# Kernel tuning notes

Measured on AMD Instinct MI355X. Metric: run time of the kernel, lower is better.

Reference implementation:

```python
import jax, jax.numpy as jnp
import numpy as np

RADIUS = 1.0
N_NORM = 1  # default n_norm in the torch module


def setup_inputs() -> dict:
    key = jax.random.key(0)
    k1, k2, k3 = jax.random.split(key, 3)
    batch, n, c_in, c_out = 8, 2048, 64, 64
    features = jax.random.normal(k1, (batch, n, c_in), dtype=jnp.float32)
    geometry = jax.random.normal(k2, (batch, n, 3), dtype=jnp.float32)
    # learned per-edge kernel weight: K(diff)[o,i] = sum_x diff[x] * Wk[x,o,i]
    Wk = jax.random.normal(k3, (3, c_out, c_in), dtype=jnp.float32) * 0.1
    return {"features": features, "geometry": geometry, "Wk": Wk}


def reference(features, geometry, Wk):
    # diff[z,a,b,:] = geometry[z,b] - geometry[z,a]   (rb - ra in the torch code)
    diff = geometry[:, None, :, :] - geometry[:, :, None, :]  # [z, a, b, 3]
    norm = jnp.sqrt(jnp.sum(diff * diff, axis=-1))            # [z, a, b]
    # Dense masked formulation: padding every point's neighbor list to k = n
    # with rel_mask zeros is mathematically identical to the torch variable-k
    # padding (masked entries contribute nothing to the einsum reduce).
    rel_mask = (norm < RADIUS).astype(features.dtype)         # [z, a, b]
    # Fused reduce. Original: einsum('zab,zabij,zabj->zai', mask, K(diff), feat[nei])
    # with K(diff)[z,a,b,i,j] = einsum('zabx,xij->zabij', diff, Wk). We contract
    # over b first to avoid materializing the [z,a,b,i,j] kernel tensor.
    s = jnp.einsum('zab,zabx,zbj->zaxj', rel_mask, diff, features)  # [z, a, 3, c_in]
    out = jnp.einsum('zaxj,xij->zai', s, Wk) / jnp.sqrt(jnp.asarray(N_NORM, features.dtype))
    return out
```

## Files before the change

kernel.cpp:

```cpp
#include <hip/hip_runtime.h>
#include <stdint.h>

#define NPTS 2048

#define BP_OFF    0ULL
#define BP_BYTES  (8ULL * 8 * 64 * 2 * 1024)
#define W2F_OFF   (BP_OFF + BP_BYTES)
#define W2F_BYTES (24ULL * 1024)
#define WXF_OFF   (W2F_OFF + W2F_BYTES)
#define WXF_BYTES (24ULL * 1024)
#define MW_OFF    (WXF_OFF + WXF_BYTES)
#define MW_BYTES  (8ULL * 32 * 64 * 256)

typedef __attribute__((ext_vector_type(8))) short bf16x8;
typedef __attribute__((ext_vector_type(4))) float f32x4;
typedef __attribute__((ext_vector_type(16))) float f32x16;
typedef __attribute__((ext_vector_type(4))) unsigned int u32x4;

__device__ __forceinline__ unsigned f2bf(float f) {
  union { float f; unsigned u; } v; v.f = f;
  return (v.u + 0x7FFFu + ((v.u >> 16) & 1u)) >> 16;
}

__device__ __forceinline__ bf16x8 pack8(const float4 a, const float4 b) {
  u32x4 r;
  r[0] = f2bf(a.x) | (f2bf(a.y) << 16);
  r[1] = f2bf(a.z) | (f2bf(a.w) << 16);
  r[2] = f2bf(b.x) | (f2bf(b.y) << 16);
  r[3] = f2bf(b.z) | (f2bf(b.w) << 16);
  union { u32x4 u; bf16x8 h; } c; c.u = r; return c.h;
}

__device__ __forceinline__ bf16x8 unpack_mask(unsigned mq) {
  const unsigned dep0 = ((mq & 15u) * 0x204081u) & 0x01010101u;
  const unsigned dep1 = (((mq >> 4) & 15u) * 0x204081u) & 0x01010101u;
  u32x4 aw;
  aw[0] = __builtin_amdgcn_perm(dep0, 0u, 0x0C050C04u) * 0x3F80u;
  aw[1] = __builtin_amdgcn_perm(dep0, 0u, 0x0C070C06u) * 0x3F80u;
  aw[2] = __builtin_amdgcn_perm(dep1, 0u, 0x0C050C04u) * 0x3F80u;
  aw[3] = __builtin_amdgcn_perm(dep1, 0u, 0x0C070C06u) * 0x3F80u;
  union { u32x4 u; bf16x8 h; } cv; cv.u = aw;
  return cv.h;
}

__global__ __launch_bounds__(256, 2) void k1_prep(const float* __restrict__ feat,
                                                  const float* __restrict__ geom,
                                                  const float* __restrict__ Wk,
                                                  unsigned char* __restrict__ ws) {
  const int blk = blockIdx.x, t = threadIdx.x;
  if (blk < 512) {
    const int z = blk >> 6, s = blk & 63;
    __shared__ float FT[64][37];
    __shared__ float g[96];
    __shared__ float gxp[2048], gyp[2048], gzp[2048];
    const float* fz = feat + ((size_t)z * NPTS + s * 32) * 64;
    const float* gz = geom + (size_t)z * NPTS * 3;
    {
      const int row = t >> 3, j0 = (t & 7) << 3;
      const float4 v0 = *(const float4*)&fz[row * 64 + j0];
      const float4 v1 = *(const float4*)&fz[row * 64 + j0 + 4];
      FT[j0 + 0][row] = v0.x; FT[j0 + 1][row] = v0.y;
      FT[j0 + 2][row] = v0.z; FT[j0 + 3][row] = v0.w;
      FT[j0 + 4][row] = v1.x; FT[j0 + 5][row] = v1.y;
      FT[j0 + 6][row] = v1.z; FT[j0 + 7][row] = v1.w;
    }
    if (t < 96) g[t] = gz[s * 96 + t];
    {
      float v[24];
#pragma unroll
      for (int i = 0; i < 6; ++i) *(float4*)&v[i * 4] = *(const float4*)&gz[t * 24 + i * 4];
#pragma unroll
      for (int i = 0; i < 8; ++i) {
        const int pp = i * 256 + t;
        gxp[pp] = v[i * 3 + 0]; gyp[pp] = v[i * 3 + 1]; gzp[pp] = v[i * 3 + 2];
      }
    }
    __syncthreads();

    {
      const int w = t >> 6, L = t & 63;
      const int nn = L >> 2, k0 = (L & 3) * 8;
      const int j = w * 16 + nn;
      float f[8];
#pragma unroll
      for (int i = 0; i < 8; ++i) f[i] = FT[j][k0 + i];
      float gx[3][8];
#pragma unroll
      for (int x = 0; x < 3; ++x)
#pragma unroll
        for (int i = 0; i < 8; ++i) gx[x][i] = g[(k0 + i) * 3 + x];
      const int kc = (L & 3) >> 1, h = (L & 3) & 1;
      const int lane16 = h * 32 + (w & 1) * 16 + nn;
      unsigned char* base = ws + BP_OFF + (size_t)z * 1048576 + (size_t)(w >> 1) * 131072 +
                            (size_t)s * 2048 + (size_t)kc * 1024 + (size_t)lane16 * 16;
#pragma unroll
      for (int it = 0; it < 4; ++it) {
        u32x4 pv;
#pragma unroll
        for (int p = 0; p < 4; ++p) {
          float f0 = f[2 * p], f1 = f[2 * p + 1];
          if (it < 3) { f0 *= gx[it][2 * p]; f1 *= gx[it][2 * p + 1]; }
          pv[p] = f2bf(f0) | (f2bf(f1) << 16);
        }
        *(u32x4*)(base + (size_t)it * 262144) = pv;
      }
    }

    {
      float ax[8], ay[8], az[8];
#pragma unroll
      for (int i = 0; i < 8; ++i) {
        const int pp = i * 256 + t;
        ax[i] = gxp[pp]; ay[i] = gyp[pp]; az[i] = gzp[pp];
      }
      unsigned bits[8] = {0, 0, 0, 0, 0, 0, 0, 0};
      for (int j = 0; j < 32; ++j) {
        const float bx = g[j * 3 + 0], by = g[j * 3 + 1], bz = g[j * 3 + 2];
#pragma unroll
        for (int i = 0; i < 8; ++i) {
          const float d0 = bx - ax[i], d1 = by - ay[i], d2 = bz - az[i];
          const float n2 = fmaf(d2, d2, fmaf(d1, d1, d0 * d0));
          bits[i] |= (n2 < 1.0f ? 1u : 0u) << j;
        }
      }
      unsigned int* mw = (unsigned int*)(ws + MW_OFF);
#pragma unroll
      for (int i = 0; i < 8; ++i) {
        const int r = t * 8 + i;
        mw[(((size_t)z * 32 + (r >> 6)) * 64 + s) * 64 + (r & 15) * 4 + ((r >> 4) & 3)] = bits[i];
      }
    }
  } else if (blk == 512) {
    for (int e = t; e < 1536; e += 256) {
      const int frag = e >> 6, lp = e & 63, nn = lp >> 2, qd = lp & 3;
      const int kb = frag >> 2, cb = frag & 3;
      u32x4 pv;
#pragma unroll
      for (int p = 0; p < 4; ++p) {
        const int k0 = kb * 32 + qd * 8 + 2 * p;
        const float v0 = Wk[(k0 >> 6) * 4096 + (cb * 16 + nn) * 64 + (k0 & 63)];
        const float v1 = Wk[((k0 + 1) >> 6) * 4096 + (cb * 16 + nn) * 64 + ((k0 + 1) & 63)];
        pv[p] = f2bf(v0) | (f2bf(v1) << 16);
      }
      *(u32x4*)(ws + W2F_OFF + (size_t)frag * 1024 + lp * 16) = pv;
    }
  } else {
    for (int e = t; e < 1536; e += 256) {
      const int frag = e >> 6, lp = e & 63, nn = lp >> 2, qd = lp & 3;
      const int kb = frag / 12, cb = frag % 12, xi = cb * 16 + nn;
      u32x4 pv;
#pragma unroll
      for (int p = 0; p < 4; ++p) {
        const int k0 = kb * 32 + qd * 8 + 2 * p;
        const float v0 = Wk[(xi >> 6) * 4096 + (xi & 63) * 64 + k0];
        const float v1 = Wk[(xi >> 6) * 4096 + (xi & 63) * 64 + k0 + 1];
        pv[p] = f2bf(v0) | (f2bf(v1) << 16);
      }
      *(u32x4*)(ws + WXF_OFF + (size_t)frag * 1024 + lp * 16) = pv;
    }
  }
}

__global__ __launch_bounds__(512, 2) void k2_gemm(const float* __restrict__ geom,
                                                  const unsigned char* __restrict__ ws,
                                                  float* __restrict__ out) {
  __shared__ __align__(16) float Ct[64 * 256];

  const int t = threadIdx.x, lane = t & 63, w = t >> 6;
  const int l31 = lane & 31;
  const int h8 = (lane >> 5) << 3;
  const int quad = (lane >> 4) & 3, n = lane & 15;
  const int fragoff = n * 64 + quad * 16;
  const int bx = blockIdx.x;
  const int z = bx & 7, at = bx >> 3, a0 = at * 64;

  const unsigned char* bpz = ws + BP_OFF + (size_t)z * 1048576 + (size_t)w * 131072;
  const unsigned char* mwz = ws + MW_OFF + ((size_t)z * 32 + at) * 16384;
  const int midx = ((l31 & 15) * 4 + (l31 >> 4)) * 4;

  f32x16 acc0, acc1;
#pragma unroll
  for (int r = 0; r < 16; ++r) { acc0[r] = 0.f; acc1[r] = 0.f; }

  bf16x8 Bf[4][2];
  unsigned Mf0[4], Mf1[4];
#pragma unroll
  for (int sl = 0; sl < 4; ++sl) {
    Bf[sl][0] = *(const bf16x8*)(bpz + (size_t)sl * 2048 + (size_t)lane * 16);
    Bf[sl][1] = *(const bf16x8*)(bpz + (size_t)sl * 2048 + 1024 + (size_t)lane * 16);
    Mf0[sl] = *(const unsigned*)(mwz + sl * 256 + midx);
    Mf1[sl] = *(const unsigned*)(mwz + sl * 256 + midx + 8);
  }

#define KSTEP(S, SL)                                                           \
  {                                                                            \
    const unsigned m0 = Mf0[SL], m1 = Mf1[SL];                                 \
    const bf16x8 A00 = unpack_mask((m0 >> h8) & 0xFFu);                        \
    const bf16x8 A10 = unpack_mask((m1 >> h8) & 0xFFu);                        \
    const bf16x8 A01 = unpack_mask((m0 >> (16 + h8)) & 0xFFu);                 \
    const bf16x8 A11 = unpack_mask((m1 >> (16 + h8)) & 0xFFu);                 \
    acc0 = __builtin_amdgcn_mfma_f32_32x32x16_bf16(A00, Bf[SL][0], acc0, 0, 0, 0); \
    acc1 = __builtin_amdgcn_mfma_f32_32x32x16_bf16(A10, Bf[SL][0], acc1, 0, 0, 0); \
    acc0 = __builtin_amdgcn_mfma_f32_32x32x16_bf16(A01, Bf[SL][1], acc0, 0, 0, 0); \
    acc1 = __builtin_amdgcn_mfma_f32_32x32x16_bf16(A11, Bf[SL][1], acc1, 0, 0, 0); \
    const int sp = (S) + 4 > 63 ? 63 : (S) + 4;                                \
    Mf0[SL] = *(const unsigned*)(mwz + sp * 256 + midx);                       \
    Mf1[SL] = *(const unsigned*)(mwz + sp * 256 + midx + 8);                   \
    Bf[SL][0] = *(const bf16x8*)(bpz + (size_t)sp * 2048 + (size_t)lane * 16); \
    Bf[SL][1] = *(const bf16x8*)(bpz + (size_t)sp * 2048 + 1024 + (size_t)lane * 16); \
  }

  for (int s4 = 0; s4 < 64; s4 += 4) {
    KSTEP(s4 + 0, 0) KSTEP(s4 + 1, 1) KSTEP(s4 + 2, 2) KSTEP(s4 + 3, 3)
  }
#undef KSTEP

  {
    const int rh = 4 * (lane >> 5);
#pragma unroll
    for (int r = 0; r < 16; ++r) {
      const int row = (r & 3) + 8 * (r >> 2) + rh;
      const int col = 32 * w + l31;
      Ct[row * 256 + (((col >> 2) ^ row) << 2) + (col & 3)] = acc0[r];
      const int row1 = row + 32;
      Ct[row1 * 256 + (((col >> 2) ^ row1) << 2) + (col & 3)] = acc1[r];
    }
  }
  __syncthreads();

  if (w < 4) {
    const int lm = 16 * w + n;
    bf16x8 Across[8];
#pragma unroll
    for (int kb = 0; kb < 8; ++kb) {
      const int c0 = (kb * 8 + quad * 2) ^ lm;
      const int c1 = (kb * 8 + quad * 2 + 1) ^ lm;
      const float4 f0 = *(const float4*)&Ct[lm * 256 + c0 * 4];
      const float4 f1 = *(const float4*)&Ct[lm * 256 + c1 * 4];
      Across[kb] = pack8(f0, f1);
    }

    f32x4 mn[4], V[12];
#pragma unroll
    for (int i = 0; i < 4; ++i)
#pragma unroll
      for (int r = 0; r < 4; ++r) mn[i][r] = 0.f;
#pragma unroll
    for (int i = 0; i < 12; ++i)
#pragma unroll
      for (int r = 0; r < 4; ++r) V[i][r] = 0.f;

    const unsigned char* w2f = ws + W2F_OFF;
    const unsigned char* wxf = ws + WXF_OFF;
#pragma unroll
    for (int kb = 0; kb < 6; ++kb)
#pragma unroll
      for (int cb = 0; cb < 4; ++cb) {
        const bf16x8 Bfr = *(const bf16x8*)(w2f + (size_t)(kb * 4 + cb) * 1024 + fragoff);
        mn[cb] = __builtin_amdgcn_mfma_f32_16x16x32_bf16(Across[kb], Bfr, mn[cb], 0, 0, 0);
      }
#pragma unroll
    for (int kb = 0; kb < 2; ++kb)
#pragma unroll
      for (int cb = 0; cb < 12; ++cb) {
        const bf16x8 Bfr = *(const bf16x8*)(wxf + (size_t)(kb * 12 + cb) * 1024 + fragoff);
        V[cb] = __builtin_amdgcn_mfma_f32_16x16x32_bf16(Across[6 + kb], Bfr, V[cb], 0, 0, 0);
      }

#pragma unroll
    for (int r = 0; r < 4; ++r) {
      const int af = a0 + 16 * w + quad * 4 + r;
      const float g0 = geom[((size_t)z * NPTS + af) * 3 + 0];
      const float g1 = geom[((size_t)z * NPTS + af) * 3 + 1];
      const float g2 = geom[((size_t)z * NPTS + af) * 3 + 2];
#pragma unroll
      for (int cb = 0; cb < 4; ++cb) {
        const float v = mn[cb][r] - g0 * V[cb][r] - g1 * V[cb + 4][r] - g2 * V[cb + 8][r];
        out[((size_t)z * NPTS + af) * 64 + cb * 16 + n] = v;
      }
    }
  }
}

extern "C" void kernel_launch(void* const* d_in, const int* in_sizes, int n_in,
                              void* d_out, int out_size, void* d_ws, size_t ws_size,
                              hipStream_t stream) {
  const float* feat = (const float*)d_in[0];
  const float* geom = (const float*)d_in[1];
  const float* Wk   = (const float*)d_in[2];
  float* out = (float*)d_out;
  unsigned char* ws = (unsigned char*)d_ws;

  k1_prep<<<dim3(514), 256, 0, stream>>>(feat, geom, Wk, ws);
  k2_gemm<<<dim3(256), 512, 0, stream>>>(geom, ws, out);
}
```

Before: 103.1 us.

## Double M tile to 128 rows and stage unpacked masks in shared memory

Each k2_gemm block now covers 128 query rows instead of 64, so every B fragment loaded from the workspace feeds four MFMA tiles instead of two. The mask bits are unpacked to bf16 cooperatively by all waves and written into double-buffered LDS tiles, which every wave then reads, replacing the per-wave redundant mask loads and unpacks. The grid halves to 128 blocks with one block per CU and a 128 KB LDS footprint. This may leave part of the 256 CUs idle and lowers occupancy, and it adds a block barrier after each group of 8 k-steps.

```diff
diff --git a/kernel.cpp b/kernel.cpp
--- a/kernel.cpp
+++ b/kernel.cpp
@@ -161,10 +161,12 @@
   }
 }
 
-__global__ __launch_bounds__(512, 2) void k2_gemm(const float* __restrict__ geom,
+__global__ __launch_bounds__(512, 1) void k2_gemm(const float* __restrict__ geom,
                                                   const unsigned char* __restrict__ ws,
                                                   float* __restrict__ out) {
-  __shared__ __align__(16) float Ct[64 * 256];
+  __shared__ __align__(16) float Ct[128 * 256];
+  unsigned char* const ab0 = (unsigned char*)Ct;
+  unsigned char* const ab1 = (unsigned char*)Ct + 65536;
 
   const int t = threadIdx.x, lane = t & 63, w = t >> 6;
   const int l31 = lane & 31;
@@ -172,69 +174,93 @@
   const int quad = (lane >> 4) & 3, n = lane & 15;
   const int fragoff = n * 64 + quad * 16;
   const int bx = blockIdx.x;
-  const int z = bx & 7, at = bx >> 3, a0 = at * 64;
+  const int z = bx & 7, at = bx >> 3, a0 = at * 128;
 
   const unsigned char* bpz = ws + BP_OFF + (size_t)z * 1048576 + (size_t)w * 131072;
-  const unsigned char* mwz = ws + MW_OFF + ((size_t)z * 32 + at) * 16384;
-  const int midx = ((l31 & 15) * 4 + (l31 >> 4)) * 4;
-
-  f32x16 acc0, acc1;
-#pragma unroll
-  for (int r = 0; r < 16; ++r) { acc0[r] = 0.f; acc1[r] = 0.f; }
+
+  const int pmt = w >> 1, pkc = w & 1;
+  const int prow = pmt * 32 + l31;
+  const int pat32 = 2 * at + (prow >> 6), pr6 = prow & 63;
+  const unsigned* mrow = (const unsigned*)(ws + MW_OFF) +
+                         (((size_t)(z * 32 + pat32)) << 12) + (pr6 & 15) * 4 + ((pr6 >> 4) & 3);
+  const int pshift = pkc * 16 + h8;
+
+  f32x16 acc[4];
+#pragma unroll
+  for (int mt = 0; mt < 4; ++mt)
+#pragma unroll
+    for (int r = 0; r < 16; ++r) acc[mt][r] = 0.f;
 
   bf16x8 Bf[4][2];
-  unsigned Mf0[4], Mf1[4];
 #pragma unroll
   for (int sl = 0; sl < 4; ++sl) {
     Bf[sl][0] = *(const bf16x8*)(bpz + (size_t)sl * 2048 + (size_t)lane * 16);
     Bf[sl][1] = *(const bf16x8*)(bpz + (size_t)sl * 2048 + 1024 + (size_t)lane * 16);
-    Mf0[sl] = *(const unsigned*)(mwz + sl * 256 + midx);
-    Mf1[sl] = *(const unsigned*)(mwz + sl * 256 + midx + 8);
-  }
-
-#define KSTEP(S, SL)                                                           \
-  {                                                                            \
-    const unsigned m0 = Mf0[SL], m1 = Mf1[SL];                                 \
-    const bf16x8 A00 = unpack_mask((m0 >> h8) & 0xFFu);                        \
-    const bf16x8 A10 = unpack_mask((m1 >> h8) & 0xFFu);                        \
-    const bf16x8 A01 = unpack_mask((m0 >> (16 + h8)) & 0xFFu);                 \
-    const bf16x8 A11 = unpack_mask((m1 >> (16 + h8)) & 0xFFu);                 \
-    acc0 = __builtin_amdgcn_mfma_f32_32x32x16_bf16(A00, Bf[SL][0], acc0, 0, 0, 0); \
-    acc1 = __builtin_amdgcn_mfma_f32_32x32x16_bf16(A10, Bf[SL][0], acc1, 0, 0, 0); \
-    acc0 = __builtin_amdgcn_mfma_f32_32x32x16_bf16(A01, Bf[SL][1], acc0, 0, 0, 0); \
-    acc1 = __builtin_amdgcn_mfma_f32_32x32x16_bf16(A11, Bf[SL][1], acc1, 0, 0, 0); \
-    const int sp = (S) + 4 > 63 ? 63 : (S) + 4;                                \
-    Mf0[SL] = *(const unsigned*)(mwz + sp * 256 + midx);                       \
-    Mf1[SL] = *(const unsigned*)(mwz + sp * 256 + midx + 8);                   \
-    Bf[SL][0] = *(const bf16x8*)(bpz + (size_t)sp * 2048 + (size_t)lane * 16); \
-    Bf[SL][1] = *(const bf16x8*)(bpz + (size_t)sp * 2048 + 1024 + (size_t)lane * 16); \
-  }
-
-  for (int s4 = 0; s4 < 64; s4 += 4) {
-    KSTEP(s4 + 0, 0) KSTEP(s4 + 1, 1) KSTEP(s4 + 2, 2) KSTEP(s4 + 3, 3)
-  }
-#undef KSTEP
+  }
+
+  unsigned M[8];
+#pragma unroll
+  for (int i = 0; i < 8; ++i) M[i] = mrow[(size_t)i * 64];
+#pragma unroll
+  for (int i = 0; i < 8; ++i)
+    *(bf16x8*)(ab0 + ((i * 8 + w) << 10) + (size_t)lane * 16) =
+        unpack_mask((M[i] >> pshift) & 0xFFu);
+  __syncthreads();
+
+  for (int g = 0; g < 8; ++g) {
+    unsigned char* const cur = (g & 1) ? ab1 : ab0;
+    unsigned char* const nxt = (g & 1) ? ab0 : ab1;
+    const int sbase = g * 8;
+    const bool prod = (g < 7);
+    if (prod) {
+#pragma unroll
+      for (int i = 0; i < 8; ++i) M[i] = mrow[(size_t)(sbase + 8 + i) * 64];
+    }
+#pragma unroll
+    for (int i = 0; i < 8; ++i) {
+      const int S = sbase + i;
+      bf16x8 Af[4][2];
+#pragma unroll
+      for (int mt = 0; mt < 4; ++mt)
+#pragma unroll
+        for (int kc = 0; kc < 2; ++kc)
+          Af[mt][kc] = *(const bf16x8*)(cur + ((i * 8 + mt * 2 + kc) << 10) + (size_t)lane * 16);
+#pragma unroll
+      for (int kc = 0; kc < 2; ++kc)
+#pragma unroll
+        for (int mt = 0; mt < 4; ++mt)
+          acc[mt] = __builtin_amdgcn_mfma_f32_32x32x16_bf16(Af[mt][kc], Bf[i & 3][kc],
+                                                            acc[mt], 0, 0, 0);
+      const int sp = S + 4 > 63 ? 63 : S + 4;
+      Bf[i & 3][0] = *(const bf16x8*)(bpz + (size_t)sp * 2048 + (size_t)lane * 16);
+      Bf[i & 3][1] = *(const bf16x8*)(bpz + (size_t)sp * 2048 + 1024 + (size_t)lane * 16);
+      if (prod)
+        *(bf16x8*)(nxt + ((i * 8 + w) << 10) + (size_t)lane * 16) =
+            unpack_mask((M[i] >> pshift) & 0xFFu);
+    }
+    __syncthreads();
+  }
 
   {
     const int rh = 4 * (lane >> 5);
-#pragma unroll
-    for (int r = 0; r < 16; ++r) {
-      const int row = (r & 3) + 8 * (r >> 2) + rh;
-      const int col = 32 * w + l31;
-      Ct[row * 256 + (((col >> 2) ^ row) << 2) + (col & 3)] = acc0[r];
-      const int row1 = row + 32;
-      Ct[row1 * 256 + (((col >> 2) ^ row1) << 2) + (col & 3)] = acc1[r];
-    }
+    const int col = 32 * w + l31;
+#pragma unroll
+    for (int mt = 0; mt < 4; ++mt)
+#pragma unroll
+      for (int r = 0; r < 16; ++r) {
+        const int row = mt * 32 + (r & 3) + 8 * (r >> 2) + rh;
+        Ct[row * 256 + (((col >> 2) ^ (row & 63)) << 2) + (col & 3)] = acc[mt][r];
+      }
   }
   __syncthreads();
 
-  if (w < 4) {
+  {
     const int lm = 16 * w + n;
     bf16x8 Across[8];
 #pragma unroll
     for (int kb = 0; kb < 8; ++kb) {
-      const int c0 = (kb * 8 + quad * 2) ^ lm;
-      const int c1 = (kb * 8 + quad * 2 + 1) ^ lm;
+      const int c0 = (kb * 8 + quad * 2) ^ (lm & 63);
+      const int c1 = (kb * 8 + quad * 2 + 1) ^ (lm & 63);
       const float4 f0 = *(const float4*)&Ct[lm * 256 + c0 * 4];
       const float4 f1 = *(const float4*)&Ct[lm * 256 + c1 * 4];
       Across[kb] = pack8(f0, f1);
@@ -292,5 +318,5 @@
   unsigned char* ws = (unsigned char*)d_ws;
 
   k1_prep<<<dim3(514), 256, 0, stream>>>(feat, geom, Wk, ws);
-  k2_gemm<<<dim3(256), 512, 0, stream>>>(geom, ws, out);
-}
+  k2_gemm<<<dim3(128), 512, 0, stream>>>(geom, ws, out);
+}
```

Result: slower. 113.7 us (+10.3%).

## Share unpacked mask A-fragments across waves via double-buffered LDS

Applied to the files above, without the earlier changes.

Instead of each of the 8 waves loading and unpacking all mask bits into bf16 A fragments itself, each wave now unpacks a slice and stores it in LDS, double-buffered in groups of 8 K-steps with a barrier per group. All waves then read the shared A fragments from LDS. This removes redundant global mask loads and unpack ALU work per wave. In exchange it adds LDS traffic and eight block-wide synchronisations, and it reuses the Ct shared buffer as staging.

```diff
diff --git a/kernel.cpp b/kernel.cpp
--- a/kernel.cpp
+++ b/kernel.cpp
@@ -165,6 +165,7 @@
                                                   const unsigned char* __restrict__ ws,
                                                   float* __restrict__ out) {
   __shared__ __align__(16) float Ct[64 * 256];
+  unsigned char* const abuf = (unsigned char*)Ct;
 
   const int t = threadIdx.x, lane = t & 63, w = t >> 6;
   const int l31 = lane & 31;
@@ -175,52 +176,69 @@
   const int z = bx & 7, at = bx >> 3, a0 = at * 64;
 
   const unsigned char* bpz = ws + BP_OFF + (size_t)z * 1048576 + (size_t)w * 131072;
-  const unsigned char* mwz = ws + MW_OFF + ((size_t)z * 32 + at) * 16384;
-  const int midx = ((l31 & 15) * 4 + (l31 >> 4)) * 4;
+
+  const int ptype = w & 3, pkc = ptype & 1;
+  const int prow = (ptype >> 1) * 32 + l31;
+  const unsigned* mrow = (const unsigned*)(ws + MW_OFF) + (((size_t)(z * 32 + at)) << 12) +
+                         (prow & 15) * 4 + ((prow >> 4) & 3);
+  const int pshift = pkc * 16 + h8;
+  const int psub = (w >> 2) * 4;
 
   f32x16 acc0, acc1;
 #pragma unroll
   for (int r = 0; r < 16; ++r) { acc0[r] = 0.f; acc1[r] = 0.f; }
 
   bf16x8 Bf[4][2];
-  unsigned Mf0[4], Mf1[4];
 #pragma unroll
   for (int sl = 0; sl < 4; ++sl) {
     Bf[sl][0] = *(const bf16x8*)(bpz + (size_t)sl * 2048 + (size_t)lane * 16);
     Bf[sl][1] = *(const bf16x8*)(bpz + (size_t)sl * 2048 + 1024 + (size_t)lane * 16);
-    Mf0[sl] = *(const unsigned*)(mwz + sl * 256 + midx);
-    Mf1[sl] = *(const unsigned*)(mwz + sl * 256 + midx + 8);
-  }
-
-#define KSTEP(S, SL)                                                           \
-  {                                                                            \
-    const unsigned m0 = Mf0[SL], m1 = Mf1[SL];                                 \
-    const bf16x8 A00 = unpack_mask((m0 >> h8) & 0xFFu);                        \
-    const bf16x8 A10 = unpack_mask((m1 >> h8) & 0xFFu);                        \
-    const bf16x8 A01 = unpack_mask((m0 >> (16 + h8)) & 0xFFu);                 \
-    const bf16x8 A11 = unpack_mask((m1 >> (16 + h8)) & 0xFFu);                 \
-    acc0 = __builtin_amdgcn_mfma_f32_32x32x16_bf16(A00, Bf[SL][0], acc0, 0, 0, 0); \
-    acc1 = __builtin_amdgcn_mfma_f32_32x32x16_bf16(A10, Bf[SL][0], acc1, 0, 0, 0); \
-    acc0 = __builtin_amdgcn_mfma_f32_32x32x16_bf16(A01, Bf[SL][1], acc0, 0, 0, 0); \
-    acc1 = __builtin_amdgcn_mfma_f32_32x32x16_bf16(A11, Bf[SL][1], acc1, 0, 0, 0); \
-    const int sp = (S) + 4 > 63 ? 63 : (S) + 4;                                \
-    Mf0[SL] = *(const unsigned*)(mwz + sp * 256 + midx);                       \
-    Mf1[SL] = *(const unsigned*)(mwz + sp * 256 + midx + 8);                   \
-    Bf[SL][0] = *(const bf16x8*)(bpz + (size_t)sp * 2048 + (size_t)lane * 16); \
-    Bf[SL][1] = *(const bf16x8*)(bpz + (size_t)sp * 2048 + 1024 + (size_t)lane * 16); \
-  }
-
-  for (int s4 = 0; s4 < 64; s4 += 4) {
-    KSTEP(s4 + 0, 0) KSTEP(s4 + 1, 1) KSTEP(s4 + 2, 2) KSTEP(s4 + 3, 3)
-  }
-#undef KSTEP
+  }
+
+  unsigned M[4];
+#pragma unroll
+  for (int j = 0; j < 4; ++j) M[j] = mrow[(size_t)(psub + j) * 64];
+#pragma unroll
+  for (int j = 0; j < 4; ++j)
+    *(bf16x8*)(abuf + (((psub + j) * 4 + ptype) << 10) + (size_t)lane * 16) =
+        unpack_mask((M[j] >> pshift) & 0xFFu);
+  __syncthreads();
+
+  for (int g = 0; g < 8; ++g) {
+    unsigned char* const cur = abuf + (size_t)(g & 1) * 32768;
+    unsigned char* const nxt = abuf + (size_t)((g & 1) ^ 1) * 32768;
+    const bool prod = (g < 7);
+    if (prod) {
+#pragma unroll
+      for (int j = 0; j < 4; ++j) M[j] = mrow[(size_t)((g + 1) * 8 + psub + j) * 64];
+    }
+#pragma unroll
+    for (int i = 0; i < 8; ++i) {
+      const int S = g * 8 + i;
+      const bf16x8 A00 = *(const bf16x8*)(cur + ((i * 4 + 0) << 10) + (size_t)lane * 16);
+      const bf16x8 A01 = *(const bf16x8*)(cur + ((i * 4 + 1) << 10) + (size_t)lane * 16);
+      const bf16x8 A10 = *(const bf16x8*)(cur + ((i * 4 + 2) << 10) + (size_t)lane * 16);
+      const bf16x8 A11 = *(const bf16x8*)(cur + ((i * 4 + 3) << 10) + (size_t)lane * 16);
+      acc0 = __builtin_amdgcn_mfma_f32_32x32x16_bf16(A00, Bf[i & 3][0], acc0, 0, 0, 0);
+      acc1 = __builtin_amdgcn_mfma_f32_32x32x16_bf16(A10, Bf[i & 3][0], acc1, 0, 0, 0);
+      acc0 = __builtin_amdgcn_mfma_f32_32x32x16_bf16(A01, Bf[i & 3][1], acc0, 0, 0, 0);
+      acc1 = __builtin_amdgcn_mfma_f32_32x32x16_bf16(A11, Bf[i & 3][1], acc1, 0, 0, 0);
+      const int sp = S + 4 > 63 ? 63 : S + 4;
+      Bf[i & 3][0] = *(const bf16x8*)(bpz + (size_t)sp * 2048 + (size_t)lane * 16);
+      Bf[i & 3][1] = *(const bf16x8*)(bpz + (size_t)sp * 2048 + 1024 + (size_t)lane * 16);
+      if (prod && i < 4)
+        *(bf16x8*)(nxt + (((psub + i) * 4 + ptype) << 10) + (size_t)lane * 16) =
+            unpack_mask((M[i] >> pshift) & 0xFFu);
+    }
+    __syncthreads();
+  }
 
   {
     const int rh = 4 * (lane >> 5);
+    const int col = 32 * w + l31;
 #pragma unroll
     for (int r = 0; r < 16; ++r) {
       const int row = (r & 3) + 8 * (r >> 2) + rh;
-      const int col = 32 * w + l31;
       Ct[row * 256 + (((col >> 2) ^ row) << 2) + (col & 3)] = acc0[r];
       const int row1 = row + 32;
       Ct[row1 * 256 + (((col >> 2) ^ row1) << 2) + (col & 3)] = acc1[r];
```

Result: faster. 95.35 us (-7.6%).
